# Performance work log

Hardware: AMD Instinct MI355X
Metric: run time of the kernel (lower is better)

The kernel has to match this reference:

```python
import jax, jax.numpy as jnp
import numpy as np

EPS = 1e-5


def setup_inputs() -> dict:
    key = jax.random.key(0)
    k_x, k_y, k_w, k_b = jax.random.split(key, 4)
    B, IN, OUT = 16384, 1024, 1024
    x = jax.random.normal(k_x, (B, IN), dtype=jnp.float32)
    y = jax.random.normal(k_y, (B, OUT), dtype=jnp.float32)
    # nn.Linear default init scale ~ 1/sqrt(in_features); keep activations sane
    weight = jax.random.normal(k_w, (OUT, IN), dtype=jnp.float32) / np.sqrt(IN)
    bias = jax.random.normal(k_b, (OUT,), dtype=jnp.float32) / np.sqrt(IN)
    gamma = jnp.ones((OUT,), dtype=jnp.float32)
    beta = jnp.zeros((OUT,), dtype=jnp.float32)
    return {"x": x, "y": y, "weight": weight, "bias": bias, "gamma": gamma, "beta": beta}


def reference(x, y, weight, bias, gamma, beta):
    # Linear: z[b, o] = sum_i x[b, i] * weight[o, i] + bias[o]
    z = jnp.einsum('bi,oi->bo', x, weight) + bias
    # LayerNorm over the feature (out_features) dim, biased variance
    mean = jnp.mean(z, axis=-1, keepdims=True)
    var = jnp.mean(jnp.square(z), axis=-1, keepdims=True) - jnp.square(mean)
    ln = (z - mean) * jax.lax.rsqrt(var + EPS) * gamma + beta
    # residual add then elementwise multiply
    return (ln + y) * y
```

## Files before the change

kernel.cpp:

```cpp
#include <hip/hip_runtime.h>
#include <stdint.h>

typedef unsigned short u16;
typedef __attribute__((ext_vector_type(8))) short short8;
typedef __attribute__((ext_vector_type(4))) float floatx4;
typedef __attribute__((ext_vector_type(2))) float floatx2;

#define K_DIM 1024
#define N_DIM 1024
#define BM 64
#define BK 32
#define NCHUNK (K_DIM / BK)
#define HCHUNK (NCHUNK / 2)

__device__ __forceinline__ u16 f2b(float f) {
    union { float f; uint32_t i; } v; v.f = f;
    uint32_t u = v.i;
    return (u16)((u + 0x7FFFu + ((u >> 16) & 1u)) >> 16);
}
__device__ __forceinline__ float b2f(u16 u) {
    union { uint32_t i; float f; } v; v.i = ((uint32_t)u) << 16; return v.f;
}

__global__ __launch_bounds__(256) void pack_w_kernel(const float* __restrict__ w,
                                                     u16* __restrict__ wpk) {
    int gid  = blockIdx.x * 256 + threadIdx.x;
    int lane = gid & 63;
    int kc   = (gid >> 6) & 31;
    int tile = gid >> 11;
    int n = tile * 16 + (lane & 15);
    int k = kc * 32 + (lane >> 4) * 8;
    const float* src = w + (size_t)n * K_DIM + k;
    floatx4 a = *(const floatx4*)(src);
    floatx4 b = *(const floatx4*)(src + 4);
    short8 o;
    o[0] = (short)f2b(a[0]); o[1] = (short)f2b(a[1]);
    o[2] = (short)f2b(a[2]); o[3] = (short)f2b(a[3]);
    o[4] = (short)f2b(b[0]); o[5] = (short)f2b(b[1]);
    o[6] = (short)f2b(b[2]); o[7] = (short)f2b(b[3]);
    *(short8*)(wpk + (size_t)gid * 8) = o;
}

__global__ __launch_bounds__(1024) void gemm_stats_kernel(
    const float* __restrict__ x, const u16* __restrict__ wpk,
    const float* __restrict__ bias, u16* __restrict__ zout,
    float* __restrict__ stats)
{
    __shared__ __align__(16) u16 lds16[HCHUNK * BM * BK];
    __shared__ __align__(16) u16 zbuf[16 * 1024];
    __shared__ float ls_sum[64];
    __shared__ float ls_sum2[64];

    const int tid  = threadIdx.x;
    const int lane = tid & 63;
    const int wv   = tid >> 6;
    const int q    = lane >> 4;
    const int row0 = blockIdx.x * BM;

    if (tid < 64) { ls_sum[tid] = 0.0f; ls_sum2[tid] = 0.0f; }

    const int sr = tid >> 4;
    const int sk = (tid & 15) << 1;
    const float* s_src = x + (size_t)(row0 + sr) * K_DIM + sk;
    const int s_qs  = (sk >> 3) ^ ((sr >> 1) & 3);
    const int s_off = sr * 64 + s_qs * 16 + (sk & 7) * 2;

    const u16* bp = wpk + (size_t)wv * 65536 + lane * 8;

    const int a_base = (lane & 15) * 64 + (q ^ (((lane & 15) >> 1) & 3)) * 16;

    floatx4 acc[4][4];
#pragma unroll
    for (int mi = 0; mi < 4; ++mi)
#pragma unroll
        for (int ni = 0; ni < 4; ++ni)
            acc[mi][ni] = (floatx4){0.0f, 0.0f, 0.0f, 0.0f};

#pragma unroll 4
    for (int c = 0; c < HCHUNK; ++c) {
        floatx2 v = *(const floatx2*)(s_src + c * BK);
        uint32_t p = (uint32_t)f2b(v[0]) | ((uint32_t)f2b(v[1]) << 16);
        *(uint32_t*)((char*)lds16 + c * 4096 + s_off) = p;
    }

    short8 bfr[2][4];
#pragma unroll
    for (int ni = 0; ni < 4; ++ni)
        bfr[0][ni] = *(const short8*)(bp + ni * 16384);

    __syncthreads();

    for (int half = 0; half < 2; ++half) {
        if (half == 1) {
            __syncthreads();
#pragma unroll 4
            for (int c = 0; c < HCHUNK; ++c) {
                floatx2 v = *(const floatx2*)(s_src + (HCHUNK + c) * BK);
                uint32_t p = (uint32_t)f2b(v[0]) | ((uint32_t)f2b(v[1]) << 16);
                *(uint32_t*)((char*)lds16 + c * 4096 + s_off) = p;
            }
            __syncthreads();
        }

#pragma unroll 2
        for (int c = 0; c < HCHUNK; ++c) {
            const int kc  = half * HCHUNK + c;
            const int cur = kc & 1;
            const int nxt = cur ^ 1;
            const char* ab = (const char*)lds16 + c * 4096;

            short8 af0 = *(const short8*)(ab + a_base);
            short8 af1 = *(const short8*)(ab + a_base + 1024);
            short8 af2 = *(const short8*)(ab + a_base + 2048);
            short8 af3 = *(const short8*)(ab + a_base + 3072);

            const int kn = (kc + 1 < NCHUNK) ? (kc + 1) : kc;
#pragma unroll
            for (int ni = 0; ni < 4; ++ni)
                bfr[nxt][ni] = *(const short8*)(bp + ni * 16384 + kn * 512);

#pragma unroll
            for (int ni = 0; ni < 4; ++ni) {
                acc[0][ni] = __builtin_amdgcn_mfma_f32_16x16x32_bf16(
                    af0, bfr[cur][ni], acc[0][ni], 0, 0, 0);
                acc[1][ni] = __builtin_amdgcn_mfma_f32_16x16x32_bf16(
                    af1, bfr[cur][ni], acc[1][ni], 0, 0, 0);
                acc[2][ni] = __builtin_amdgcn_mfma_f32_16x16x32_bf16(
                    af2, bfr[cur][ni], acc[2][ni], 0, 0, 0);
                acc[3][ni] = __builtin_amdgcn_mfma_f32_16x16x32_bf16(
                    af3, bfr[cur][ni], acc[3][ni], 0, 0, 0);
            }
        }
    }

    float bias_v[4];
#pragma unroll
    for (int ni = 0; ni < 4; ++ni)
        bias_v[ni] = bias[(wv << 6) + (ni << 4) + (lane & 15)];
#pragma unroll
    for (int mi = 0; mi < 4; ++mi)
#pragma unroll
        for (int ni = 0; ni < 4; ++ni)
#pragma unroll
            for (int r = 0; r < 4; ++r)
                acc[mi][ni][r] += bias_v[ni];

    __syncthreads();

#pragma unroll
    for (int mi = 0; mi < 4; ++mi)
#pragma unroll
        for (int r = 0; r < 4; ++r) {
            float s = 0.0f, s2 = 0.0f;
#pragma unroll
            for (int ni = 0; ni < 4; ++ni) {
                float v = acc[mi][ni][r];
                s += v; s2 += v * v;
            }
#pragma unroll
            for (int m = 1; m < 16; m <<= 1) {
                s  += __shfl_xor(s,  m, 64);
                s2 += __shfl_xor(s2, m, 64);
            }
            if ((lane & 15) == 0) {
                int rl = (mi << 4) + (q << 2) + r;
                atomicAdd(&ls_sum[rl], s);
                atomicAdd(&ls_sum2[rl], s2);
            }
        }

    __syncthreads();
    if (tid < 64) {
        float mean = ls_sum[tid] * (1.0f / 1024.0f);
        float var  = ls_sum2[tid] * (1.0f / 1024.0f) - mean * mean;
        stats[row0 + tid]           = mean;
        stats[16384 + row0 + tid]   = rsqrtf(var + 1e-5f);
    }

    for (int mi = 0; mi < 4; ++mi) {
#pragma unroll
        for (int ni = 0; ni < 4; ++ni)
#pragma unroll
            for (int r = 0; r < 4; ++r) {
                int lr   = (q << 2) + r;
                int lin  = (((wv << 6) + (ni << 4) + (lane & 15)) << 1);
                int phys = lr * 2048 + (lin ^ (q << 5));
                *(u16*)((char*)zbuf + phys) = f2b(acc[mi][ni][r]);
            }
        __syncthreads();
#pragma unroll
        for (int it = 0; it < 2; ++it) {
            int row  = (tid >> 7) + (it << 3);
            int c8   = tid & 127;
            int phys = row * 2048 + ((c8 << 4) ^ (((row >> 2) & 3) << 5));
            short8 z8 = *(const short8*)((const char*)zbuf + phys);
            int grow  = row0 + (mi << 4) + row;
            *(short8*)(zout + (size_t)grow * N_DIM + c8 * 8) = z8;
        }
        __syncthreads();
    }
}

__global__ __launch_bounds__(256) void ln_apply_kernel(
    const u16* __restrict__ z, const float* __restrict__ y,
    const float* __restrict__ stats, const float* __restrict__ gamma,
    const float* __restrict__ beta, float* __restrict__ out)
{
    int g   = blockIdx.x * 256 + threadIdx.x;
    int row = g >> 7;
    int c8  = g & 127;
    float mean = stats[row];
    float rs   = stats[16384 + row];
    short8 z8 = *(const short8*)(z + (size_t)row * N_DIM + c8 * 8);
    const float* yp  = y     + (size_t)row * N_DIM + c8 * 8;
    const float* gp  = gamma + c8 * 8;
    const float* bpv = beta  + c8 * 8;
    float*       op  = out   + (size_t)row * N_DIM + c8 * 8;
    floatx4 y0 = *(const floatx4*)(yp);
    floatx4 y1 = *(const floatx4*)(yp + 4);
    floatx4 g0 = *(const floatx4*)(gp);
    floatx4 g1 = *(const floatx4*)(gp + 4);
    floatx4 b0 = *(const floatx4*)(bpv);
    floatx4 b1 = *(const floatx4*)(bpv + 4);
    floatx4 o0, o1;
#pragma unroll
    for (int e = 0; e < 4; ++e) {
        float zv = b2f((u16)z8[e]);
        o0[e] = ((zv - mean) * rs * g0[e] + b0[e] + y0[e]) * y0[e];
    }
#pragma unroll
    for (int e = 0; e < 4; ++e) {
        float zv = b2f((u16)z8[e + 4]);
        o1[e] = ((zv - mean) * rs * g1[e] + b1[e] + y1[e]) * y1[e];
    }
    *(floatx4*)(op)     = o0;
    *(floatx4*)(op + 4) = o1;
}

__global__ __launch_bounds__(1024) void fused_gemm_ln_kernel(
    const float* __restrict__ x, const float* __restrict__ y,
    const u16* __restrict__ wpk, const float* __restrict__ bias,
    const float* __restrict__ gamma, const float* __restrict__ beta,
    float* __restrict__ out)
{
    __shared__ __align__(16) u16 lds16[HCHUNK * BM * BK];
    __shared__ __align__(16) u16 zbuf[16 * 1024];
    __shared__ float ls_sum[64];
    __shared__ float ls_sum2[64];
    __shared__ float ls_mean[64];
    __shared__ float ls_rs[64];

    const int tid  = threadIdx.x;
    const int lane = tid & 63;
    const int wv   = tid >> 6;
    const int q    = lane >> 4;
    const int row0 = blockIdx.x * BM;

    if (tid < 64) { ls_sum[tid] = 0.0f; ls_sum2[tid] = 0.0f; }

    const int sr = tid >> 4;
    const int sk = (tid & 15) << 1;
    const float* s_src = x + (size_t)(row0 + sr) * K_DIM + sk;
    const int s_qs  = (sk >> 3) ^ ((sr >> 1) & 3);
    const int s_off = sr * 64 + s_qs * 16 + (sk & 7) * 2;

    const u16* bp = wpk + (size_t)wv * 65536 + lane * 8;
    const int a_base = (lane & 15) * 64 + (q ^ (((lane & 15) >> 1) & 3)) * 16;

    floatx4 acc[4][4];
#pragma unroll
    for (int mi = 0; mi < 4; ++mi)
#pragma unroll
        for (int ni = 0; ni < 4; ++ni)
            acc[mi][ni] = (floatx4){0.0f, 0.0f, 0.0f, 0.0f};

#pragma unroll 4
    for (int c = 0; c < HCHUNK; ++c) {
        floatx2 v = *(const floatx2*)(s_src + c * BK);
        uint32_t p = (uint32_t)f2b(v[0]) | ((uint32_t)f2b(v[1]) << 16);
        *(uint32_t*)((char*)lds16 + c * 4096 + s_off) = p;
    }
    short8 bfr[2][4];
#pragma unroll
    for (int ni = 0; ni < 4; ++ni)
        bfr[0][ni] = *(const short8*)(bp + ni * 16384);
    __syncthreads();

    for (int half = 0; half < 2; ++half) {
        if (half == 1) {
            __syncthreads();
#pragma unroll 4
            for (int c = 0; c < HCHUNK; ++c) {
                floatx2 v = *(const floatx2*)(s_src + (HCHUNK + c) * BK);
                uint32_t p = (uint32_t)f2b(v[0]) | ((uint32_t)f2b(v[1]) << 16);
                *(uint32_t*)((char*)lds16 + c * 4096 + s_off) = p;
            }
            __syncthreads();
        }
#pragma unroll 2
        for (int c = 0; c < HCHUNK; ++c) {
            const int kc  = half * HCHUNK + c;
            const int cur = kc & 1;
            const int nxt = cur ^ 1;
            const char* ab = (const char*)lds16 + c * 4096;
            short8 af0 = *(const short8*)(ab + a_base);
            short8 af1 = *(const short8*)(ab + a_base + 1024);
            short8 af2 = *(const short8*)(ab + a_base + 2048);
            short8 af3 = *(const short8*)(ab + a_base + 3072);
            const int kn = (kc + 1 < NCHUNK) ? (kc + 1) : kc;
#pragma unroll
            for (int ni = 0; ni < 4; ++ni)
                bfr[nxt][ni] = *(const short8*)(bp + ni * 16384 + kn * 512);
#pragma unroll
            for (int ni = 0; ni < 4; ++ni) {
                acc[0][ni] = __builtin_amdgcn_mfma_f32_16x16x32_bf16(
                    af0, bfr[cur][ni], acc[0][ni], 0, 0, 0);
                acc[1][ni] = __builtin_amdgcn_mfma_f32_16x16x32_bf16(
                    af1, bfr[cur][ni], acc[1][ni], 0, 0, 0);
                acc[2][ni] = __builtin_amdgcn_mfma_f32_16x16x32_bf16(
                    af2, bfr[cur][ni], acc[2][ni], 0, 0, 0);
                acc[3][ni] = __builtin_amdgcn_mfma_f32_16x16x32_bf16(
                    af3, bfr[cur][ni], acc[3][ni], 0, 0, 0);
            }
        }
    }

    float bias_v[4];
#pragma unroll
    for (int ni = 0; ni < 4; ++ni)
        bias_v[ni] = bias[(wv << 6) + (ni << 4) + (lane & 15)];
#pragma unroll
    for (int mi = 0; mi < 4; ++mi)
#pragma unroll
        for (int ni = 0; ni < 4; ++ni)
#pragma unroll
            for (int r = 0; r < 4; ++r)
                acc[mi][ni][r] += bias_v[ni];

    __syncthreads();

#pragma unroll
    for (int mi = 0; mi < 4; ++mi)
#pragma unroll
        for (int r = 0; r < 4; ++r) {
            float s = 0.0f, s2 = 0.0f;
#pragma unroll
            for (int ni = 0; ni < 4; ++ni) {
                float v = acc[mi][ni][r];
                s += v; s2 += v * v;
            }
#pragma unroll
            for (int m = 1; m < 16; m <<= 1) {
                s  += __shfl_xor(s,  m, 64);
                s2 += __shfl_xor(s2, m, 64);
            }
            if ((lane & 15) == 0) {
                int rl = (mi << 4) + (q << 2) + r;
                atomicAdd(&ls_sum[rl], s);
                atomicAdd(&ls_sum2[rl], s2);
            }
        }

    __syncthreads();
    if (tid < 64) {
        float mean = ls_sum[tid] * (1.0f / 1024.0f);
        float var  = ls_sum2[tid] * (1.0f / 1024.0f) - mean * mean;
        ls_mean[tid] = mean;
        ls_rs[tid]   = rsqrtf(var + 1e-5f);
    }

    for (int mi = 0; mi < 4; ++mi) {
#pragma unroll
        for (int ni = 0; ni < 4; ++ni)
#pragma unroll
            for (int r = 0; r < 4; ++r) {
                int lr   = (q << 2) + r;
                int lin  = (((wv << 6) + (ni << 4) + (lane & 15)) << 1);
                int phys = lr * 2048 + (lin ^ (q << 5));
                *(u16*)((char*)zbuf + phys) = f2b(acc[mi][ni][r]);
            }
        __syncthreads();
#pragma unroll
        for (int it = 0; it < 2; ++it) {
            int row  = (tid >> 7) + (it << 3);
            int c8   = tid & 127;
            int phys = row * 2048 + ((c8 << 4) ^ (((row >> 2) & 3) << 5));
            short8 z8 = *(const short8*)((const char*)zbuf + phys);
            int grow  = row0 + (mi << 4) + row;
            float mean = ls_mean[(mi << 4) + row];
            float rs   = ls_rs[(mi << 4) + row];
            const float* yp = y     + (size_t)grow * N_DIM + c8 * 8;
            const float* gp = gamma + c8 * 8;
            const float* bpv = beta + c8 * 8;
            float*       op = out   + (size_t)grow * N_DIM + c8 * 8;
            floatx4 y0 = *(const floatx4*)(yp);
            floatx4 y1 = *(const floatx4*)(yp + 4);
            floatx4 g0 = *(const floatx4*)(gp);
            floatx4 g1 = *(const floatx4*)(gp + 4);
            floatx4 b0 = *(const floatx4*)(bpv);
            floatx4 b1 = *(const floatx4*)(bpv + 4);
            floatx4 o0, o1;
#pragma unroll
            for (int e = 0; e < 4; ++e) {
                float zv = b2f((u16)z8[e]);
                o0[e] = ((zv - mean) * rs * g0[e] + b0[e] + y0[e]) * y0[e];
            }
#pragma unroll
            for (int e = 0; e < 4; ++e) {
                float zv = b2f((u16)z8[e + 4]);
                o1[e] = ((zv - mean) * rs * g1[e] + b1[e] + y1[e]) * y1[e];
            }
            *(floatx4*)(op)     = o0;
            *(floatx4*)(op + 4) = o1;
        }
        __syncthreads();
    }
}

extern "C" void kernel_launch(void* const* d_in, const int* in_sizes, int n_in,
                              void* d_out, int out_size, void* d_ws, size_t ws_size,
                              hipStream_t stream) {
    const float* x     = (const float*)d_in[0];
    const float* y     = (const float*)d_in[1];
    const float* wgt   = (const float*)d_in[2];
    const float* bias  = (const float*)d_in[3];
    const float* gamma = (const float*)d_in[4];
    const float* beta  = (const float*)d_in[5];
    float* out = (float*)d_out;

    u16* wpk = (u16*)d_ws;
    const size_t WPK_BYTES   = 2u * 1024u * 1024u;
    const size_t STATS_BYTES = 128u * 1024u;
    const size_t Z_BYTES     = 32u * 1024u * 1024u;
    const int M = in_sizes[0] / K_DIM;

    pack_w_kernel<<<512, 256, 0, stream>>>(wgt, wpk);

    if (ws_size >= WPK_BYTES + STATS_BYTES + Z_BYTES) {
        float* stats = (float*)((char*)d_ws + WPK_BYTES);
        u16*   zws   = (u16*)((char*)d_ws + WPK_BYTES + STATS_BYTES);
        gemm_stats_kernel<<<M / BM, 1024, 0, stream>>>(x, wpk, bias, zws, stats);
        ln_apply_kernel<<<M * (N_DIM / 8) / 256, 256, 0, stream>>>(
            zws, y, stats, gamma, beta, out);
    } else {
        fused_gemm_ln_kernel<<<M / BM, 1024, 0, stream>>>(
            x, y, wpk, bias, gamma, beta, out);
    }
}
```

Measured before the change: 225.6 us.

## Retile GEMM to 256x256 blocks with LDS-staged double-buffered A/B and atomic row stats

Replaces the 64-row full-width GEMM block with 256x256 output tiles over 512 threads, staging both bf16 x and packed weights in double-buffered LDS and prefetching the next k-group into registers. Each x tile is now converted once and shared across 256 columns rather than each wave streaming its own weight slice from global memory, which raises arithmetic intensity. Because a block no longer sees a full row, per-row sum and sum-of-squares are accumulated with global atomics into a memset buffer, and mean/rstd are computed in the apply kernel. This adds a memset launch, global atomics and a large 128KB+ LDS footprint that limits occupancy to one block per CU.

```diff
diff --git a/kernel.cpp b/kernel.cpp
--- a/kernel.cpp
+++ b/kernel.cpp
@@ -8,10 +8,12 @@
 
 #define K_DIM 1024
 #define N_DIM 1024
+#define BK 32
+#define NCHUNK 32
+#define GCH 2
+#define NGRP (NCHUNK / GCH)
 #define BM 64
-#define BK 32
-#define NCHUNK (K_DIM / BK)
-#define HCHUNK (NCHUNK / 2)
+#define HCHUNK 16
 
 __device__ __forceinline__ u16 f2b(float f) {
     union { float f; uint32_t i; } v; v.f = f;
@@ -41,119 +43,146 @@
     *(short8*)(wpk + (size_t)gid * 8) = o;
 }
 
-__global__ __launch_bounds__(1024) void gemm_stats_kernel(
+__global__ __launch_bounds__(512) void gemm256_kernel(
     const float* __restrict__ x, const u16* __restrict__ wpk,
     const float* __restrict__ bias, u16* __restrict__ zout,
-    float* __restrict__ stats)
+    float* __restrict__ gsum, float* __restrict__ gsum2)
 {
-    __shared__ __align__(16) u16 lds16[HCHUNK * BM * BK];
-    __shared__ __align__(16) u16 zbuf[16 * 1024];
-    __shared__ float ls_sum[64];
-    __shared__ float ls_sum2[64];
+    __shared__ __align__(16) u16 smem[65536];
+    __shared__ float ls_sum[256];
+    __shared__ float ls_sum2[256];
 
     const int tid  = threadIdx.x;
     const int lane = tid & 63;
     const int wv   = tid >> 6;
+    const int wr   = wv >> 1;
+    const int wc   = wv & 1;
     const int q    = lane >> 4;
-    const int row0 = blockIdx.x * BM;
-
-    if (tid < 64) { ls_sum[tid] = 0.0f; ls_sum2[tid] = 0.0f; }
-
-    const int sr = tid >> 4;
-    const int sk = (tid & 15) << 1;
-    const float* s_src = x + (size_t)(row0 + sr) * K_DIM + sk;
-    const int s_qs  = (sk >> 3) ^ ((sr >> 1) & 3);
-    const int s_off = sr * 64 + s_qs * 16 + (sk & 7) * 2;
-
-    const u16* bp = wpk + (size_t)wv * 65536 + lane * 8;
+    const int rb   = blockIdx.x >> 2;
+    const int cb   = blockIdx.x & 3;
+    const int row0 = rb * 256;
+    const int col0 = cb * 256;
+
+    if (tid < 256) { ls_sum[tid] = 0.0f; ls_sum2[tid] = 0.0f; }
+
+    const int rb8 = tid >> 4;
+    const int sk  = (tid & 15) << 1;
+    const int s_qs  = (sk >> 3) ^ ((rb8 >> 1) & 3);
+    const int s_off0 = rb8 * 64 + s_qs * 16 + (sk & 7) * 2;
+    const int s_off1 = s_off0 + 2048;
+    const float* xb = x + (size_t)(row0 + rb8) * K_DIM + sk;
+
+    const u16* wb0 = wpk + ((size_t)(cb * 16 + wv * 2) * 32) * 512 + lane * 8;
+    const u16* wb1 = wpk + ((size_t)(cb * 16 + wv * 2 + 1) * 32) * 512 + lane * 8;
 
     const int a_base = (lane & 15) * 64 + (q ^ (((lane & 15) >> 1) & 3)) * 16;
 
-    floatx4 acc[4][4];
-#pragma unroll
-    for (int mi = 0; mi < 4; ++mi)
-#pragma unroll
-        for (int ni = 0; ni < 4; ++ni)
+    floatx4 acc[4][8];
+#pragma unroll
+    for (int mi = 0; mi < 4; ++mi)
+#pragma unroll
+        for (int ni = 0; ni < 8; ++ni)
             acc[mi][ni] = (floatx4){0.0f, 0.0f, 0.0f, 0.0f};
 
-#pragma unroll 4
-    for (int c = 0; c < HCHUNK; ++c) {
-        floatx2 v = *(const floatx2*)(s_src + c * BK);
-        uint32_t p = (uint32_t)f2b(v[0]) | ((uint32_t)f2b(v[1]) << 16);
-        *(uint32_t*)((char*)lds16 + c * 4096 + s_off) = p;
-    }
-
-    short8 bfr[2][4];
-#pragma unroll
-    for (int ni = 0; ni < 4; ++ni)
-        bfr[0][ni] = *(const short8*)(bp + ni * 16384);
-
+    {
+        char* A0 = (char*)smem;
+        char* B0 = (char*)smem + 65536;
+#pragma unroll
+        for (int c2 = 0; c2 < GCH; ++c2) {
+#pragma unroll
+            for (int j = 0; j < 8; ++j) {
+                floatx2 v = *(const floatx2*)(xb + (size_t)((j & 1) * 32 + (j >> 1) * 64) * K_DIM + c2 * BK);
+                uint32_t p = (uint32_t)f2b(v[0]) | ((uint32_t)f2b(v[1]) << 16);
+                *(uint32_t*)(A0 + c2 * 16384 + (j >> 1) * 4096 + ((j & 1) ? s_off1 : s_off0)) = p;
+            }
+            short8 t0 = *(const short8*)(wb0 + (size_t)c2 * 512);
+            short8 t1 = *(const short8*)(wb1 + (size_t)c2 * 512);
+            *(short8*)(B0 + c2 * 16384 + (wv * 2) * 1024 + lane * 16)     = t0;
+            *(short8*)(B0 + c2 * 16384 + (wv * 2 + 1) * 1024 + lane * 16) = t1;
+        }
+    }
     __syncthreads();
 
-    for (int half = 0; half < 2; ++half) {
-        if (half == 1) {
-            __syncthreads();
-#pragma unroll 4
-            for (int c = 0; c < HCHUNK; ++c) {
-                floatx2 v = *(const floatx2*)(s_src + (HCHUNK + c) * BK);
-                uint32_t p = (uint32_t)f2b(v[0]) | ((uint32_t)f2b(v[1]) << 16);
-                *(uint32_t*)((char*)lds16 + c * 4096 + s_off) = p;
-            }
-            __syncthreads();
-        }
-
-#pragma unroll 2
-        for (int c = 0; c < HCHUNK; ++c) {
-            const int kc  = half * HCHUNK + c;
-            const int cur = kc & 1;
-            const int nxt = cur ^ 1;
-            const char* ab = (const char*)lds16 + c * 4096;
-
-            short8 af0 = *(const short8*)(ab + a_base);
-            short8 af1 = *(const short8*)(ab + a_base + 1024);
-            short8 af2 = *(const short8*)(ab + a_base + 2048);
-            short8 af3 = *(const short8*)(ab + a_base + 3072);
-
-            const int kn = (kc + 1 < NCHUNK) ? (kc + 1) : kc;
-#pragma unroll
-            for (int ni = 0; ni < 4; ++ni)
-                bfr[nxt][ni] = *(const short8*)(bp + ni * 16384 + kn * 512);
-
-#pragma unroll
-            for (int ni = 0; ni < 4; ++ni) {
-                acc[0][ni] = __builtin_amdgcn_mfma_f32_16x16x32_bf16(
-                    af0, bfr[cur][ni], acc[0][ni], 0, 0, 0);
-                acc[1][ni] = __builtin_amdgcn_mfma_f32_16x16x32_bf16(
-                    af1, bfr[cur][ni], acc[1][ni], 0, 0, 0);
-                acc[2][ni] = __builtin_amdgcn_mfma_f32_16x16x32_bf16(
-                    af2, bfr[cur][ni], acc[2][ni], 0, 0, 0);
-                acc[3][ni] = __builtin_amdgcn_mfma_f32_16x16x32_bf16(
-                    af3, bfr[cur][ni], acc[3][ni], 0, 0, 0);
-            }
-        }
-    }
-
-    float bias_v[4];
-#pragma unroll
-    for (int ni = 0; ni < 4; ++ni)
-        bias_v[ni] = bias[(wv << 6) + (ni << 4) + (lane & 15)];
-#pragma unroll
-    for (int mi = 0; mi < 4; ++mi)
-#pragma unroll
-        for (int ni = 0; ni < 4; ++ni)
+    floatx2 va[GCH][8];
+    short8  bs[GCH][2];
+
+#pragma unroll 1
+    for (int g = 0; g < NGRP; ++g) {
+        const int cur = g & 1;
+        const int nxt = cur ^ 1;
+        const bool pf = (g + 1 < NGRP);
+
+        if (pf) {
+            const int kb = (g + 1) * GCH;
+#pragma unroll
+            for (int c2 = 0; c2 < GCH; ++c2) {
+#pragma unroll
+                for (int j = 0; j < 8; ++j)
+                    va[c2][j] = *(const floatx2*)(xb + (size_t)((j & 1) * 32 + (j >> 1) * 64) * K_DIM + (kb + c2) * BK);
+                bs[c2][0] = *(const short8*)(wb0 + (size_t)(kb + c2) * 512);
+                bs[c2][1] = *(const short8*)(wb1 + (size_t)(kb + c2) * 512);
+            }
+        }
+
+#pragma unroll
+        for (int c2 = 0; c2 < GCH; ++c2) {
+            const char* Ab = (const char*)smem + cur * 32768 + c2 * 16384;
+            const char* Bb = (const char*)smem + 65536 + cur * 32768 + c2 * 16384;
+            short8 af[4];
+#pragma unroll
+            for (int mi = 0; mi < 4; ++mi)
+                af[mi] = *(const short8*)(Ab + wr * 4096 + a_base + mi * 1024);
+            short8 bf[8];
+#pragma unroll
+            for (int ni = 0; ni < 8; ++ni)
+                bf[ni] = *(const short8*)(Bb + (wc * 8 + ni) * 1024 + lane * 16);
+#pragma unroll
+            for (int mi = 0; mi < 4; ++mi)
+#pragma unroll
+                for (int ni = 0; ni < 8; ++ni)
+                    acc[mi][ni] = __builtin_amdgcn_mfma_f32_16x16x32_bf16(
+                        af[mi], bf[ni], acc[mi][ni], 0, 0, 0);
+        }
+
+        if (pf) {
+            char* An = (char*)smem + nxt * 32768;
+            char* Bn = (char*)smem + 65536 + nxt * 32768;
+#pragma unroll
+            for (int c2 = 0; c2 < GCH; ++c2) {
+#pragma unroll
+                for (int j = 0; j < 8; ++j) {
+                    uint32_t p = (uint32_t)f2b(va[c2][j][0]) | ((uint32_t)f2b(va[c2][j][1]) << 16);
+                    *(uint32_t*)(An + c2 * 16384 + (j >> 1) * 4096 + ((j & 1) ? s_off1 : s_off0)) = p;
+                }
+                *(short8*)(Bn + c2 * 16384 + (wv * 2) * 1024 + lane * 16)     = bs[c2][0];
+                *(short8*)(Bn + c2 * 16384 + (wv * 2 + 1) * 1024 + lane * 16) = bs[c2][1];
+            }
+        }
+
+        asm volatile("s_waitcnt lgkmcnt(0)" ::: "memory");
+        __builtin_amdgcn_s_barrier();
+        asm volatile("" ::: "memory");
+    }
+
+    float bias_v[8];
+#pragma unroll
+    for (int ni = 0; ni < 8; ++ni)
+        bias_v[ni] = bias[col0 + wc * 128 + ni * 16 + (lane & 15)];
+#pragma unroll
+    for (int mi = 0; mi < 4; ++mi)
+#pragma unroll
+        for (int ni = 0; ni < 8; ++ni)
 #pragma unroll
             for (int r = 0; r < 4; ++r)
                 acc[mi][ni][r] += bias_v[ni];
 
-    __syncthreads();
-
 #pragma unroll
     for (int mi = 0; mi < 4; ++mi)
 #pragma unroll
         for (int r = 0; r < 4; ++r) {
             float s = 0.0f, s2 = 0.0f;
 #pragma unroll
-            for (int ni = 0; ni < 4; ++ni) {
+            for (int ni = 0; ni < 8; ++ni) {
                 float v = acc[mi][ni][r];
                 s += v; s2 += v * v;
             }
@@ -163,39 +192,41 @@
                 s2 += __shfl_xor(s2, m, 64);
             }
             if ((lane & 15) == 0) {
-                int rl = (mi << 4) + (q << 2) + r;
+                int rl = wr * 64 + mi * 16 + (q << 2) + r;
                 atomicAdd(&ls_sum[rl], s);
                 atomicAdd(&ls_sum2[rl], s2);
             }
         }
 
     __syncthreads();
-    if (tid < 64) {
-        float mean = ls_sum[tid] * (1.0f / 1024.0f);
-        float var  = ls_sum2[tid] * (1.0f / 1024.0f) - mean * mean;
-        stats[row0 + tid]           = mean;
-        stats[16384 + row0 + tid]   = rsqrtf(var + 1e-5f);
-    }
-
-    for (int mi = 0; mi < 4; ++mi) {
-#pragma unroll
-        for (int ni = 0; ni < 4; ++ni)
-#pragma unroll
-            for (int r = 0; r < 4; ++r) {
-                int lr   = (q << 2) + r;
-                int lin  = (((wv << 6) + (ni << 4) + (lane & 15)) << 1);
-                int phys = lr * 2048 + (lin ^ (q << 5));
-                *(u16*)((char*)zbuf + phys) = f2b(acc[mi][ni][r]);
-            }
+    if (tid < 256) {
+        atomicAdd(&gsum[row0 + tid],  ls_sum[tid]);
+        atomicAdd(&gsum2[row0 + tid], ls_sum2[tid]);
+    }
+
+    char* zb = (char*)smem;
+    for (int s4 = 0; s4 < 4; ++s4) {
+        if (wr == s4) {
+#pragma unroll
+            for (int mi = 0; mi < 4; ++mi)
+#pragma unroll
+                for (int ni = 0; ni < 8; ++ni)
+#pragma unroll
+                    for (int r = 0; r < 4; ++r) {
+                        int lr  = mi * 16 + (q << 2) + r;
+                        int col = wc * 128 + ni * 16 + (lane & 15);
+                        int phys = lr * 512 + ((col << 1) ^ (q << 5));
+                        *(u16*)(zb + phys) = f2b(acc[mi][ni][r]);
+                    }
+        }
         __syncthreads();
 #pragma unroll
-        for (int it = 0; it < 2; ++it) {
-            int row  = (tid >> 7) + (it << 3);
-            int c8   = tid & 127;
-            int phys = row * 2048 + ((c8 << 4) ^ (((row >> 2) & 3) << 5));
-            short8 z8 = *(const short8*)((const char*)zbuf + phys);
-            int grow  = row0 + (mi << 4) + row;
-            *(short8*)(zout + (size_t)grow * N_DIM + c8 * 8) = z8;
+        for (int it = 0; it < 4; ++it) {
+            int row = tid >> 3;
+            int c8  = (tid & 7) + it * 8;
+            int phys = row * 512 + ((c8 << 4) ^ (((row >> 2) & 3) << 5));
+            short8 z8 = *(const short8*)(zb + phys);
+            *(short8*)(zout + (size_t)(row0 + s4 * 64 + row) * N_DIM + col0 + c8 * 8) = z8;
         }
         __syncthreads();
     }
@@ -209,8 +240,11 @@
     int g   = blockIdx.x * 256 + threadIdx.x;
     int row = g >> 7;
     int c8  = g & 127;
-    float mean = stats[row];
-    float rs   = stats[16384 + row];
+    float s  = stats[row];
+    float s2 = stats[16384 + row];
+    float mean = s * (1.0f / 1024.0f);
+    float var  = s2 * (1.0f / 1024.0f) - mean * mean;
+    float rs   = rsqrtf(var + 1e-5f);
     short8 z8 = *(const short8*)(z + (size_t)row * N_DIM + c8 * 8);
     const float* yp  = y     + (size_t)row * N_DIM + c8 * 8;
     const float* gp  = gamma + c8 * 8;
@@ -313,14 +347,10 @@
                 bfr[nxt][ni] = *(const short8*)(bp + ni * 16384 + kn * 512);
 #pragma unroll
             for (int ni = 0; ni < 4; ++ni) {
-                acc[0][ni] = __builtin_amdgcn_mfma_f32_16x16x32_bf16(
-                    af0, bfr[cur][ni], acc[0][ni], 0, 0, 0);
-                acc[1][ni] = __builtin_amdgcn_mfma_f32_16x16x32_bf16(
-                    af1, bfr[cur][ni], acc[1][ni], 0, 0, 0);
-                acc[2][ni] = __builtin_amdgcn_mfma_f32_16x16x32_bf16(
-                    af2, bfr[cur][ni], acc[2][ni], 0, 0, 0);
-                acc[3][ni] = __builtin_amdgcn_mfma_f32_16x16x32_bf16(
-                    af3, bfr[cur][ni], acc[3][ni], 0, 0, 0);
+                acc[0][ni] = __builtin_amdgcn_mfma_f32_16x16x32_bf16(af0, bfr[cur][ni], acc[0][ni], 0, 0, 0);
+                acc[1][ni] = __builtin_amdgcn_mfma_f32_16x16x32_bf16(af1, bfr[cur][ni], acc[1][ni], 0, 0, 0);
+                acc[2][ni] = __builtin_amdgcn_mfma_f32_16x16x32_bf16(af2, bfr[cur][ni], acc[2][ni], 0, 0, 0);
+                acc[3][ni] = __builtin_amdgcn_mfma_f32_16x16x32_bf16(af3, bfr[cur][ni], acc[3][ni], 0, 0, 0);
             }
         }
     }
@@ -439,7 +469,9 @@
     if (ws_size >= WPK_BYTES + STATS_BYTES + Z_BYTES) {
         float* stats = (float*)((char*)d_ws + WPK_BYTES);
         u16*   zws   = (u16*)((char*)d_ws + WPK_BYTES + STATS_BYTES);
-        gemm_stats_kernel<<<M / BM, 1024, 0, stream>>>(x, wpk, bias, zws, stats);
+        hipMemsetAsync(stats, 0, STATS_BYTES, stream);
+        gemm256_kernel<<<(M / 256) * 4, 512, 0, stream>>>(
+            x, wpk, bias, zws, stats, stats + 16384);
         ln_apply_kernel<<<M * (N_DIM / 8) / 256, 256, 0, stream>>>(
             zws, y, stats, gamma, beta, out);
     } else {
```

Result: no change. 226.9 us (+0.6%).
